# Optimization experiments

Measured on AMD Instinct MI355X. Metric: run time of the kernel, lower is better.

The kernel has to match this reference:

```python
import jax, jax.numpy as jnp
import numpy as np

N_NODES = 50000
N_EDGES = 800000
NODE_DIM = 128
EDGE_DIM = 32
HID = 64
NEG_SLOPE = 0.2  # PyG GATConv default


def _gat_layer(x, src, dst, edge_attr, W, We, a_src, a_dst, a_edge, b, n_nodes):
    """PyG GATConv with heads=1, add_self_loops=True, fill_value='mean'."""
    h = x @ W                      # [N, H] node transform (bias=False in PyG)
    he = edge_attr @ We            # [E, H] edge transform
    # self-loop edge attr = mean of incoming edge_attr per node; linearity lets
    # us take the segment-mean of the transformed he instead.
    deg = jax.ops.segment_sum(jnp.ones((src.shape[0],), h.dtype), dst, num_segments=n_nodes)
    he_loop = jax.ops.segment_sum(he, dst, num_segments=n_nodes) / jnp.maximum(deg, 1.0)[:, None]
    loop = jnp.arange(n_nodes)
    src_a = jnp.concatenate([src, loop])
    dst_a = jnp.concatenate([dst, loop])
    he_a = jnp.concatenate([he, he_loop], axis=0)
    s_src = h @ a_src              # [N]
    s_dst = h @ a_dst              # [N]
    logits = jax.nn.leaky_relu(s_src[src_a] + s_dst[dst_a] + he_a @ a_edge, NEG_SLOPE)
    # segment softmax over destination nodes (every node has a self loop)
    m = jax.ops.segment_max(logits, dst_a, num_segments=n_nodes)
    ex = jnp.exp(logits - m[dst_a])
    denom = jax.ops.segment_sum(ex, dst_a, num_segments=n_nodes)
    alpha = ex / denom[dst_a]
    out = jax.ops.segment_sum(alpha[:, None] * h[src_a], dst_a, num_segments=n_nodes)
    return out + b


def setup_inputs() -> dict:
    key = jax.random.key(0)
    ks = jax.random.split(key, 20)
    s = 0.05
    inp = {
        "x": jax.random.normal(ks[0], (N_NODES, NODE_DIM), jnp.float32),
        "edge_index": jax.random.randint(ks[1], (2, N_EDGES), 0, N_NODES, jnp.int64 if jax.config.jax_enable_x64 else jnp.int32).astype(jnp.int32),
        "edge_attr": jax.random.normal(ks[2], (N_EDGES, EDGE_DIM), jnp.float32),
        "W1": jax.random.normal(ks[3], (NODE_DIM, HID)) * s,
        "We1": jax.random.normal(ks[4], (EDGE_DIM, HID)) * s,
        "as1": jax.random.normal(ks[5], (HID,)) * s,
        "ad1": jax.random.normal(ks[6], (HID,)) * s,
        "ae1": jax.random.normal(ks[7], (HID,)) * s,
        "b1": jnp.zeros((HID,)),
        "W2": jax.random.normal(ks[8], (HID, HID)) * s,
        "We2": jax.random.normal(ks[9], (EDGE_DIM, HID)) * s,
        "as2": jax.random.normal(ks[10], (HID,)) * s,
        "ad2": jax.random.normal(ks[11], (HID,)) * s,
        "ae2": jax.random.normal(ks[12], (HID,)) * s,
        "b2": jnp.zeros((HID,)),
        "Wc1": jax.random.normal(ks[13], (2 * HID + EDGE_DIM, HID)) * s,
        "bc1": jnp.zeros((HID,)),
        "Wc2": jax.random.normal(ks[14], (HID, 1)) * s,
        "bc2": jnp.zeros((1,)),
    }
    return inp


def reference(x, edge_index, edge_attr, W1, We1, as1, ad1, ae1, b1,
              W2, We2, as2, ad2, ae2, b2, Wc1, bc1, Wc2, bc2):
    n_nodes = x.shape[0]
    row, col = edge_index[0], edge_index[1]
    x1 = jax.nn.relu(_gat_layer(x, row, col, edge_attr, W1, We1, as1, ad1, ae1, b1, n_nodes))
    x2 = jax.nn.relu(_gat_layer(x1, row, col, edge_attr, W2, We2, as2, ad2, ae2, b2, n_nodes))
    ef = jnp.concatenate([x2[row], x2[col], edge_attr], axis=-1)  # [E, 2H+De]
    h = jax.nn.relu(ef @ Wc1 + bc1)
    return (h @ Wc2 + bc2)[:, 0]
```

## Files before the change

### kernel.cpp

```cpp
#include <hip/hip_runtime.h>
#include <hip/hip_bf16.h>

#define NODE_DIM 128
#define EDGE_DIM 32
#define HID 64
#define NEG_SLOPE 0.2f

typedef __attribute__((ext_vector_type(8))) short bf16x8;
typedef __attribute__((ext_vector_type(4))) float f32x4;


template <int CTRL, int RM, int BM>
__device__ __forceinline__ float dpp_mov(float v) {
    return __int_as_float(__builtin_amdgcn_update_dpp(
        __float_as_int(v), __float_as_int(v), CTRL, RM, BM, false));
}

__device__ __forceinline__ float wave_sum63(float v) {
    v += dpp_mov<0x111, 0xf, 0xf>(v);
    v += dpp_mov<0x112, 0xf, 0xf>(v);
    v += dpp_mov<0x114, 0xf, 0xe>(v);
    v += dpp_mov<0x118, 0xf, 0xc>(v);
    v += dpp_mov<0x142, 0xa, 0xf>(v);
    v += dpp_mov<0x143, 0xc, 0xf>(v);
    return v;
}

__device__ __forceinline__ float row16_sum15(float v) {
    v += dpp_mov<0x111, 0xf, 0xf>(v);
    v += dpp_mov<0x112, 0xf, 0xf>(v);
    v += dpp_mov<0x114, 0xf, 0xe>(v);
    v += dpp_mov<0x118, 0xf, 0xc>(v);
    return v;
}

__device__ __forceinline__ float bcast63(float v) {
    return __int_as_float(__builtin_amdgcn_readlane(__float_as_int(v), 63));
}

__device__ __forceinline__ unsigned short f2bf(float f) {
    unsigned u = __float_as_uint(f);
    unsigned r = (u + 0x7fffu + ((u >> 16) & 1u)) >> 16;
    return (unsigned short)r;
}
__device__ __forceinline__ float bf2f(unsigned short h) {
    return __uint_as_float(((unsigned)h) << 16);
}


__global__ void k_count_rank_t12(const int* __restrict__ col, int* __restrict__ deg,
                                 int* __restrict__ rank, const float* __restrict__ ea,
                                 const float* __restrict__ wea1,
                                 const float* __restrict__ wea2,
                                 float2* __restrict__ t12, int E) {
    int e = blockIdx.x * 256 + threadIdx.x;
    if (e >= E) return;
    rank[e] = atomicAdd(&deg[col[e]], 1);
    const float4* e4 = (const float4*)(ea + (size_t)e * EDGE_DIM);
    const float4* w1 = (const float4*)wea1;
    const float4* w2 = (const float4*)wea2;
    float t1 = 0.f, t2 = 0.f;
#pragma unroll
    for (int k = 0; k < EDGE_DIM / 4; k++) {
        float4 v = e4[k], a = w1[k], b = w2[k];
        t1 += v.x * a.x + v.y * a.y + v.z * a.z + v.w * a.w;
        t2 += v.x * b.x + v.y * b.y + v.z * b.z + v.w * b.w;
    }
    t12[e] = make_float2(t1, t2);
}

#define SCAN_B 256
__global__ void k_scan1(const int* __restrict__ deg, int* __restrict__ tmp,
                        int* __restrict__ bsum, int N) {
    __shared__ int s[SCAN_B];
    int i = blockIdx.x * SCAN_B + threadIdx.x;
    int v = (i < N) ? deg[i] : 0;
    s[threadIdx.x] = v;
    __syncthreads();
    for (int o = 1; o < SCAN_B; o <<= 1) {
        int t = (threadIdx.x >= o) ? s[threadIdx.x - o] : 0;
        __syncthreads();
        s[threadIdx.x] += t;
        __syncthreads();
    }
    if (i < N) tmp[i] = s[threadIdx.x];
    if (threadIdx.x == SCAN_B - 1) bsum[blockIdx.x] = s[threadIdx.x];
}

__global__ void k_scan2(int* __restrict__ bsum, int nb) {
    __shared__ int s[SCAN_B];
    int v = (threadIdx.x < nb) ? bsum[threadIdx.x] : 0;
    s[threadIdx.x] = v;
    __syncthreads();
    for (int o = 1; o < SCAN_B; o <<= 1) {
        int t = (threadIdx.x >= o) ? s[threadIdx.x - o] : 0;
        __syncthreads();
        s[threadIdx.x] += t;
        __syncthreads();
    }
    if (threadIdx.x < nb) bsum[threadIdx.x] = s[threadIdx.x] - v;
}

__global__ void k_scan3(const int* __restrict__ tmp, const int* __restrict__ deg,
                        const int* __restrict__ bsum, int* __restrict__ off, int N) {
    int i = blockIdx.x * SCAN_B + threadIdx.x;
    if (i < N) off[i] = tmp[i] - deg[i] + bsum[blockIdx.x];
}

__global__ void k_wea2(const float* __restrict__ We1, const float* __restrict__ ae1,
                       const float* __restrict__ We2, const float* __restrict__ ae2,
                       float* __restrict__ wea1, float* __restrict__ wea2) {
    int t = threadIdx.x;
    const float* We = (t < 32) ? We1 : We2;
    const float* ae = (t < 32) ? ae1 : ae2;
    float* o = (t < 32) ? wea1 : wea2;
    int k = t & 31;
    float s = 0.f;
#pragma unroll
    for (int j = 0; j < HID; j++) s += We[k * HID + j] * ae[j];
    o[k] = s;
}

__global__ void k_fill_pack(const int* __restrict__ row, const int* __restrict__ col,
                            const int* __restrict__ off, const int* __restrict__ rank,
                            const float2* __restrict__ t12, const float* __restrict__ ss1,
                            float4* __restrict__ pk, int E) {
    int e = blockIdx.x * 256 + threadIdx.x;
    if (e >= E) return;
    int dn = col[e];
    int p = off[dn] + rank[e];
    float2 t = t12[e];
    int sr = row[e];
    pk[p] = make_float4(t.x, t.y, __int_as_float(sr), t.x + ss1[sr]);
}

template <int K, int NT, bool ATT, bool PQ>
__global__ __launch_bounds__(256) void k_gemm_mfma(
    const float* __restrict__ X, const float* __restrict__ W,
    const float* __restrict__ as_, const float* __restrict__ ad_,
    unsigned short* __restrict__ H, unsigned short* __restrict__ H2,
    float* __restrict__ ss, float* __restrict__ sd, int N) {
    constexpr int KC = K / 32;
    int wv = threadIdx.x >> 6, lane = threadIdx.x & 63;
    int g = lane >> 4, li = lane & 15;
    bf16x8 bhi[KC][NT], blo[KC][NT];
#pragma unroll
    for (int c = 0; c < KC; c++)
#pragma unroll
        for (int t = 0; t < NT; t++)
#pragma unroll
            for (int j = 0; j < 8; j++) {
                int k = 32 * c + 8 * g + j;
                size_t idx = (size_t)(k + ((PQ && t >= 4) ? HID : 0)) * HID + 16 * (t & 3) + li;
                float w = W[idx];
                unsigned short h = f2bf(w);
                bhi[c][t][j] = (short)h;
                blo[c][t][j] = (short)f2bf(w - bf2f(h));
            }
    float asl[NT], adl[NT];
    if (ATT) {
#pragma unroll
        for (int t = 0; t < NT; t++) {
            asl[t] = as_[16 * t + li];
            adl[t] = ad_[16 * t + li];
        }
    }
    int ntile = (N + 15) >> 4;
    for (int tb = blockIdx.x * 4 + wv; tb < ntile; tb += gridDim.x * 4) {
        int node = tb * 16 + li;
        if (node >= N) node = N - 1;
        const float* xrow = X + (size_t)node * K;
        bf16x8 ahi[KC], alo[KC];
#pragma unroll
        for (int c = 0; c < KC; c++) {
            float4 a0 = *(const float4*)(xrow + 32 * c + 8 * g);
            float4 a1 = *(const float4*)(xrow + 32 * c + 8 * g + 4);
            float xv[8] = {a0.x, a0.y, a0.z, a0.w, a1.x, a1.y, a1.z, a1.w};
#pragma unroll
            for (int j = 0; j < 8; j++) {
                unsigned short h = f2bf(xv[j]);
                ahi[c][j] = (short)h;
                alo[c][j] = (short)f2bf(xv[j] - bf2f(h));
            }
        }
        f32x4 acc[NT];
#pragma unroll
        for (int t = 0; t < NT; t++) acc[t] = (f32x4){0.f, 0.f, 0.f, 0.f};
#pragma unroll
        for (int c = 0; c < KC; c++) {
#pragma unroll
            for (int t = 0; t < NT; t++)
                acc[t] = __builtin_amdgcn_mfma_f32_16x16x32_bf16(ahi[c], bhi[c][t], acc[t], 0, 0, 0);
#pragma unroll
            for (int t = 0; t < NT; t++)
                acc[t] = __builtin_amdgcn_mfma_f32_16x16x32_bf16(ahi[c], blo[c][t], acc[t], 0, 0, 0);
#pragma unroll
            for (int t = 0; t < NT; t++)
                acc[t] = __builtin_amdgcn_mfma_f32_16x16x32_bf16(alo[c], bhi[c][t], acc[t], 0, 0, 0);
        }
        int nbase = tb * 16 + 4 * g;
#pragma unroll
        for (int t = 0; t < NT; t++) {
            unsigned short* dst = (PQ && t >= 4) ? H2 : H;
            int cofs = 16 * (t & 3) + li;
#pragma unroll
            for (int r = 0; r < 4; r++) {
                int n = nbase + r;
                if (n < N) dst[(size_t)n * HID + cofs] = f2bf(acc[t][r]);
            }
        }
        if (ATT) {
#pragma unroll
            for (int r = 0; r < 4; r++) {
                float s1 = 0.f, s2 = 0.f;
#pragma unroll
                for (int t = 0; t < NT; t++) {
                    s1 += acc[t][r] * asl[t];
                    s2 += acc[t][r] * adl[t];
                }
                s1 = row16_sum15(s1);
                s2 = row16_sum15(s2);
                int n = nbase + r;
                if (li == 15 && n < N) {
                    ss[n] = s1;
                    sd[n] = s2;
                }
            }
        }
    }
}

template <bool FOLD>
__global__ __launch_bounds__(256) void k_aggregate(
    const unsigned short* __restrict__ H, const float* __restrict__ ss,
    const float* __restrict__ sd, const float4* __restrict__ pk,
    const int* __restrict__ off, const int* __restrict__ deg,
    const float* __restrict__ b, float* __restrict__ Xo, int N) {
    __shared__ __align__(16) float2 sh[4][64];
    int wv = threadIdx.x >> 6, lane = threadIdx.x & 63;
    int g = lane >> 4, li = lane & 15;
    int n = blockIdx.x * 4 + wv;
    if (n >= N) return;
    int st = off[n], d = deg[n];
    float sdn = sd[n];
    float tsum = 0.f, dsum = 0.f;
    float a0 = 0.f, a1 = 0.f, a2 = 0.f, a3 = 0.f;
    for (int base = 0; base < d; base += 64) {
        int i = base + lane;
        float w = 0.f;
        int s = 0;
        if (i < d) {
            float4 p = pk[st + i];
            s = __float_as_int(p.z);
            float z;
            if (FOLD) {
                tsum += p.x;
                z = p.w + sdn;
            } else {
                tsum += p.y;
                z = ss[s] + sdn + p.y;
            }
            float l = z > 0.f ? z : NEG_SLOPE * z;
            w = __expf(l);
            dsum += w;
        }
        sh[wv][lane] = make_float2(w, __int_as_float(s));
        int cnt = d - base;
        if (cnt > 64) cnt = 64;
        for (int j = 0; j < cnt; j += 4) {
            int jg = j + g;
            float2 pr = (jg < cnt) ? sh[wv][jg] : make_float2(0.f, 0.f);
            const ushort4 hv =
                *(const ushort4*)(H + (size_t)__float_as_int(pr.y) * HID + 4 * li);
            a0 += pr.x * bf2f(hv.x);
            a1 += pr.x * bf2f(hv.y);
            a2 += pr.x * bf2f(hv.z);
            a3 += pr.x * bf2f(hv.w);
        }
    }
    tsum = bcast63(wave_sum63(tsum));
    dsum = bcast63(wave_sum63(dsum));
    float tloop = tsum / (float)(d > 1 ? d : 1);
    float zs = ss[n] + sdn + tloop;
    float lself = zs > 0.f ? zs : NEG_SLOPE * zs;
    float wself = __expf(lself);
    dsum += wself;
    if (g == 0) {
        const ushort4 hv = *(const ushort4*)(H + (size_t)n * HID + 4 * li);
        a0 += wself * bf2f(hv.x);
        a1 += wself * bf2f(hv.y);
        a2 += wself * bf2f(hv.z);
        a3 += wself * bf2f(hv.w);
    }
    a0 += __shfl_xor(a0, 16, 64); a0 += __shfl_xor(a0, 32, 64);
    a1 += __shfl_xor(a1, 16, 64); a1 += __shfl_xor(a1, 32, 64);
    a2 += __shfl_xor(a2, 16, 64); a2 += __shfl_xor(a2, 32, 64);
    a3 += __shfl_xor(a3, 16, 64); a3 += __shfl_xor(a3, 32, 64);
    if (g == 0) {
        float4 bv = *(const float4*)(b + 4 * li);
        float4 o;
        o.x = fmaxf(a0 / dsum + bv.x, 0.f);
        o.y = fmaxf(a1 / dsum + bv.y, 0.f);
        o.z = fmaxf(a2 / dsum + bv.z, 0.f);
        o.w = fmaxf(a3 / dsum + bv.w, 0.f);
        *(float4*)(Xo + (size_t)n * HID + 4 * li) = o;
    }
}

__global__ __launch_bounds__(256) void k_edge_final_mfma(
    const unsigned short* __restrict__ P, const unsigned short* __restrict__ Q,
    const float* __restrict__ ea, const int* __restrict__ row,
    const int* __restrict__ col, const float* __restrict__ Wc1,
    const float* __restrict__ bc1, const float* __restrict__ Wc2,
    const float* __restrict__ bc2, float* __restrict__ out, int E) {
    int wv = threadIdx.x >> 6, lane = threadIdx.x & 63;
    int g = lane >> 4, li = lane & 15;
    bf16x8 bfrag[4];
#pragma unroll
    for (int t = 0; t < 4; t++) {
#pragma unroll
        for (int j = 0; j < 8; j++)
            bfrag[t][j] = (short)f2bf(Wc1[(size_t)(2 * HID + 8 * g + j) * HID + 4 * li + t]);
    }
    float bcv[4], wc2v[4];
#pragma unroll
    for (int t = 0; t < 4; t++) {
        bcv[t] = bc1[4 * li + t];
        wc2v[t] = Wc2[4 * li + t];
    }
    float bc2v = bc2[0];
    int ntile = (E + 15) >> 4;
    for (int tb = blockIdx.x * 4 + wv; tb < ntile; tb += gridDim.x * 4) {
        int eb = tb << 4;
        int ae_e = eb + li;
        if (ae_e >= E) ae_e = E - 1;
        const float4* ap = (const float4*)(ea + (size_t)ae_e * EDGE_DIM + 8 * g);
        float4 a0 = ap[0], a1 = ap[1];
        bf16x8 afrag;
        afrag[0] = (short)f2bf(a0.x); afrag[1] = (short)f2bf(a0.y);
        afrag[2] = (short)f2bf(a0.z); afrag[3] = (short)f2bf(a0.w);
        afrag[4] = (short)f2bf(a1.x); afrag[5] = (short)f2bf(a1.y);
        afrag[6] = (short)f2bf(a1.z); afrag[7] = (short)f2bf(a1.w);
        f32x4 acc[4];
#pragma unroll
        for (int t = 0; t < 4; t++) {
            f32x4 z = {0.f, 0.f, 0.f, 0.f};
            acc[t] = __builtin_amdgcn_mfma_f32_16x16x32_bf16(afrag, bfrag[t], z, 0, 0, 0);
        }
        int e0 = eb + 4 * g;
        int rr[4], cc[4];
        if (e0 + 3 < E) {
            int4 rv = *(const int4*)(row + e0);
            int4 cv = *(const int4*)(col + e0);
            rr[0] = rv.x; rr[1] = rv.y; rr[2] = rv.z; rr[3] = rv.w;
            cc[0] = cv.x; cc[1] = cv.y; cc[2] = cv.z; cc[3] = cv.w;
        } else {
            for (int r = 0; r < 4; r++) {
                int e = e0 + r; if (e >= E) e = E - 1;
                rr[r] = row[e]; cc[r] = col[e];
            }
        }
        float pe[4];
#pragma unroll
        for (int r = 0; r < 4; r++) {
            const ushort4 pv = *(const ushort4*)(P + (size_t)rr[r] * HID + 4 * li);
            const ushort4 qv = *(const ushort4*)(Q + (size_t)cc[r] * HID + 4 * li);
            float h0 = acc[0][r] + bf2f(pv.x) + bf2f(qv.x) + bcv[0];
            float h1 = acc[1][r] + bf2f(pv.y) + bf2f(qv.y) + bcv[1];
            float h2 = acc[2][r] + bf2f(pv.z) + bf2f(qv.z) + bcv[2];
            float h3 = acc[3][r] + bf2f(pv.w) + bf2f(qv.w) + bcv[3];
            pe[r] = fmaxf(h0, 0.f) * wc2v[0] + fmaxf(h1, 0.f) * wc2v[1] +
                    fmaxf(h2, 0.f) * wc2v[2] + fmaxf(h3, 0.f) * wc2v[3];
        }
#pragma unroll
        for (int r = 0; r < 4; r++) pe[r] = row16_sum15(pe[r]);
        if (li == 15) {
            if (e0 + 3 < E) {
                *(float4*)(out + e0) =
                    make_float4(pe[0] + bc2v, pe[1] + bc2v, pe[2] + bc2v, pe[3] + bc2v);
            } else {
                for (int r = 0; r < 4; r++)
                    if (e0 + r < E) out[e0 + r] = pe[r] + bc2v;
            }
        }
    }
}


extern "C" void kernel_launch(void* const* d_in, const int* in_sizes, int n_in,
                              void* d_out, int out_size, void* d_ws, size_t ws_size,
                              hipStream_t stream) {
    const float* x = (const float*)d_in[0];
    const int* eidx = (const int*)d_in[1];
    const float* ea = (const float*)d_in[2];
    const float* W1 = (const float*)d_in[3];
    const float* We1 = (const float*)d_in[4];
    const float* as1 = (const float*)d_in[5];
    const float* ad1 = (const float*)d_in[6];
    const float* ae1 = (const float*)d_in[7];
    const float* b1 = (const float*)d_in[8];
    const float* W2 = (const float*)d_in[9];
    const float* We2 = (const float*)d_in[10];
    const float* as2 = (const float*)d_in[11];
    const float* ad2 = (const float*)d_in[12];
    const float* ae2 = (const float*)d_in[13];
    const float* b2 = (const float*)d_in[14];
    const float* Wc1 = (const float*)d_in[15];
    const float* bc1 = (const float*)d_in[16];
    const float* Wc2 = (const float*)d_in[17];
    const float* bc2 = (const float*)d_in[18];
    float* out = (float*)d_out;

    const int N = in_sizes[0] / NODE_DIM;
    const int E = in_sizes[1] / 2;
    const int* row = eidx;
    const int* col = eidx + E;

    char* ws = (char*)d_ws;
    size_t o = 0;
    auto carve = [&](size_t bytes) -> char* {
        char* p = ws + o;
        o += (bytes + 255) & ~(size_t)255;
        return p;
    };
    int* deg = (int*)carve((size_t)N * 4);
    int* off = (int*)carve((size_t)N * 4);
    int* tmp = (int*)carve((size_t)N * 4);
    int* bsum = (int*)carve(SCAN_B * 4);
    int* rank = (int*)carve((size_t)E * 4);
    float2* t12 = (float2*)carve((size_t)E * 8);
    float4* pk12 = (float4*)carve((size_t)E * 16);
    float* wea1 = (float*)carve(EDGE_DIM * 4);
    float* wea2 = (float*)carve(EDGE_DIM * 4);
    float* ssrc = (float*)carve((size_t)N * 4);
    float* sdst = (float*)carve((size_t)N * 4);
    unsigned short* hbuf = (unsigned short*)carve((size_t)N * HID * 2);
    unsigned short* pbuf = (unsigned short*)carve((size_t)N * HID * 2);
    float* x1 = (float*)carve((size_t)N * HID * 4);
    float* x2 = (float*)carve((size_t)N * HID * 4);
    (void)ws_size;

    const int gE = (E + 255) / 256;
    const int gN256 = (N + SCAN_B - 1) / SCAN_B;
    const int gN4 = (N + 3) / 4;
    const int gT = ((N + 15) / 16 + 3) / 4;

    (void)hipMemsetAsync(deg, 0, (size_t)N * 4, stream);
    k_wea2<<<1, 64, 0, stream>>>(We1, ae1, We2, ae2, wea1, wea2);
    k_count_rank_t12<<<gE, 256, 0, stream>>>(col, deg, rank, ea, wea1, wea2, t12, E);
    k_scan1<<<gN256, SCAN_B, 0, stream>>>(deg, tmp, bsum, N);
    k_scan2<<<1, SCAN_B, 0, stream>>>(bsum, gN256);
    k_scan3<<<gN256, SCAN_B, 0, stream>>>(tmp, deg, bsum, off, N);

    k_gemm_mfma<NODE_DIM, 4, true, false><<<gT, 256, 0, stream>>>(
        x, W1, as1, ad1, hbuf, nullptr, ssrc, sdst, N);
    k_fill_pack<<<gE, 256, 0, stream>>>(row, col, off, rank, t12, ssrc, pk12, E);

    k_aggregate<true><<<gN4, 256, 0, stream>>>(hbuf, ssrc, sdst, pk12, off, deg, b1, x1, N);

    k_gemm_mfma<HID, 4, true, false><<<gT, 256, 0, stream>>>(
        x1, W2, as2, ad2, hbuf, nullptr, ssrc, sdst, N);
    k_aggregate<false><<<gN4, 256, 0, stream>>>(hbuf, ssrc, sdst, pk12, off, deg, b2, x2, N);

    k_gemm_mfma<HID, 8, false, true><<<gT, 256, 0, stream>>>(
        x2, Wc1, nullptr, nullptr, pbuf, hbuf, nullptr, nullptr, N);
    k_edge_final_mfma<<<2048, 256, 0, stream>>>(pbuf, hbuf, ea, row, col, Wc1, bc1, Wc2, bc2, out, E);
}
```

Baseline: 413.4 us.

## Move edge-attr projection into fill kernel and prefetch next tile in edge MLP

```diff
diff --git a/kernel.cpp b/kernel.cpp
--- a/kernel.cpp
+++ b/kernel.cpp
@@ -48,25 +48,11 @@
 }
 
 
-__global__ void k_count_rank_t12(const int* __restrict__ col, int* __restrict__ deg,
-                                 int* __restrict__ rank, const float* __restrict__ ea,
-                                 const float* __restrict__ wea1,
-                                 const float* __restrict__ wea2,
-                                 float2* __restrict__ t12, int E) {
+__global__ void k_count_rank(const int* __restrict__ col, int* __restrict__ deg,
+                             int* __restrict__ rank, int E) {
     int e = blockIdx.x * 256 + threadIdx.x;
     if (e >= E) return;
     rank[e] = atomicAdd(&deg[col[e]], 1);
-    const float4* e4 = (const float4*)(ea + (size_t)e * EDGE_DIM);
-    const float4* w1 = (const float4*)wea1;
-    const float4* w2 = (const float4*)wea2;
-    float t1 = 0.f, t2 = 0.f;
-#pragma unroll
-    for (int k = 0; k < EDGE_DIM / 4; k++) {
-        float4 v = e4[k], a = w1[k], b = w2[k];
-        t1 += v.x * a.x + v.y * a.y + v.z * a.z + v.w * a.w;
-        t2 += v.x * b.x + v.y * b.y + v.z * b.z + v.w * b.w;
-    }
-    t12[e] = make_float2(t1, t2);
 }
 
 #define SCAN_B 256
@@ -121,17 +107,27 @@
     o[k] = s;
 }
 
-__global__ void k_fill_pack(const int* __restrict__ row, const int* __restrict__ col,
-                            const int* __restrict__ off, const int* __restrict__ rank,
-                            const float2* __restrict__ t12, const float* __restrict__ ss1,
-                            float4* __restrict__ pk, int E) {
+__global__ void k_t12_fill(const int* __restrict__ row, const int* __restrict__ col,
+                           const int* __restrict__ off, const int* __restrict__ rank,
+                           const float* __restrict__ ea, const float* __restrict__ wea1,
+                           const float* __restrict__ wea2, const float* __restrict__ ss1,
+                           float4* __restrict__ pk, int E) {
     int e = blockIdx.x * 256 + threadIdx.x;
     if (e >= E) return;
+    const float4* e4 = (const float4*)(ea + (size_t)e * EDGE_DIM);
+    const float4* w1 = (const float4*)wea1;
+    const float4* w2 = (const float4*)wea2;
+    float t1 = 0.f, t2 = 0.f;
+#pragma unroll
+    for (int k = 0; k < EDGE_DIM / 4; k++) {
+        float4 v = e4[k], a = w1[k], b = w2[k];
+        t1 += v.x * a.x + v.y * a.y + v.z * a.z + v.w * a.w;
+        t2 += v.x * b.x + v.y * b.y + v.z * b.z + v.w * b.w;
+    }
     int dn = col[e];
     int p = off[dn] + rank[e];
-    float2 t = t12[e];
     int sr = row[e];
-    pk[p] = make_float4(t.x, t.y, __int_as_float(sr), t.x + ss1[sr]);
+    pk[p] = make_float4(t1, t2, __int_as_float(sr), t1 + ss1[sr]);
 }
 
 template <int K, int NT, bool ATT, bool PQ>
@@ -330,25 +326,19 @@
     }
     float bc2v = bc2[0];
     int ntile = (E + 15) >> 4;
-    for (int tb = blockIdx.x * 4 + wv; tb < ntile; tb += gridDim.x * 4) {
+    int stride = gridDim.x * 4;
+    int tb = blockIdx.x * 4 + wv;
+    if (tb >= ntile) return;
+
+    float4 a0, a1;
+    int rr[4], cc[4];
+    {
         int eb = tb << 4;
         int ae_e = eb + li;
         if (ae_e >= E) ae_e = E - 1;
         const float4* ap = (const float4*)(ea + (size_t)ae_e * EDGE_DIM + 8 * g);
-        float4 a0 = ap[0], a1 = ap[1];
-        bf16x8 afrag;
-        afrag[0] = (short)f2bf(a0.x); afrag[1] = (short)f2bf(a0.y);
-        afrag[2] = (short)f2bf(a0.z); afrag[3] = (short)f2bf(a0.w);
-        afrag[4] = (short)f2bf(a1.x); afrag[5] = (short)f2bf(a1.y);
-        afrag[6] = (short)f2bf(a1.z); afrag[7] = (short)f2bf(a1.w);
-        f32x4 acc[4];
-#pragma unroll
-        for (int t = 0; t < 4; t++) {
-            f32x4 z = {0.f, 0.f, 0.f, 0.f};
-            acc[t] = __builtin_amdgcn_mfma_f32_16x16x32_bf16(afrag, bfrag[t], z, 0, 0, 0);
-        }
+        a0 = ap[0]; a1 = ap[1];
         int e0 = eb + 4 * g;
-        int rr[4], cc[4];
         if (e0 + 3 < E) {
             int4 rv = *(const int4*)(row + e0);
             int4 cv = *(const int4*)(col + e0);
@@ -360,15 +350,59 @@
                 rr[r] = row[e]; cc[r] = col[e];
             }
         }
+    }
+
+    while (true) {
+        int e0 = (tb << 4) + 4 * g;
+        ushort4 pv[4], qv[4];
+#pragma unroll
+        for (int r = 0; r < 4; r++) {
+            pv[r] = *(const ushort4*)(P + (size_t)rr[r] * HID + 4 * li);
+            qv[r] = *(const ushort4*)(Q + (size_t)cc[r] * HID + 4 * li);
+        }
+        int tn = tb + stride;
+        bool hasnext = tn < ntile;
+        float4 n0 = a0, n1 = a1;
+        int nr[4], nc[4];
+#pragma unroll
+        for (int r = 0; r < 4; r++) { nr[r] = rr[r]; nc[r] = cc[r]; }
+        if (hasnext) {
+            int eb = tn << 4;
+            int ae_e = eb + li;
+            if (ae_e >= E) ae_e = E - 1;
+            const float4* ap = (const float4*)(ea + (size_t)ae_e * EDGE_DIM + 8 * g);
+            n0 = ap[0]; n1 = ap[1];
+            int ne0 = eb + 4 * g;
+            if (ne0 + 3 < E) {
+                int4 rv = *(const int4*)(row + ne0);
+                int4 cv = *(const int4*)(col + ne0);
+                nr[0] = rv.x; nr[1] = rv.y; nr[2] = rv.z; nr[3] = rv.w;
+                nc[0] = cv.x; nc[1] = cv.y; nc[2] = cv.z; nc[3] = cv.w;
+            } else {
+                for (int r = 0; r < 4; r++) {
+                    int e = ne0 + r; if (e >= E) e = E - 1;
+                    nr[r] = row[e]; nc[r] = col[e];
+                }
+            }
+        }
+        bf16x8 afrag;
+        afrag[0] = (short)f2bf(a0.x); afrag[1] = (short)f2bf(a0.y);
+        afrag[2] = (short)f2bf(a0.z); afrag[3] = (short)f2bf(a0.w);
+        afrag[4] = (short)f2bf(a1.x); afrag[5] = (short)f2bf(a1.y);
+        afrag[6] = (short)f2bf(a1.z); afrag[7] = (short)f2bf(a1.w);
+        f32x4 acc[4];
+#pragma unroll
+        for (int t = 0; t < 4; t++) {
+            f32x4 z = {0.f, 0.f, 0.f, 0.f};
+            acc[t] = __builtin_amdgcn_mfma_f32_16x16x32_bf16(afrag, bfrag[t], z, 0, 0, 0);
+        }
         float pe[4];
 #pragma unroll
         for (int r = 0; r < 4; r++) {
-            const ushort4 pv = *(const ushort4*)(P + (size_t)rr[r] * HID + 4 * li);
-            const ushort4 qv = *(const ushort4*)(Q + (size_t)cc[r] * HID + 4 * li);
-            float h0 = acc[0][r] + bf2f(pv.x) + bf2f(qv.x) + bcv[0];
-            float h1 = acc[1][r] + bf2f(pv.y) + bf2f(qv.y) + bcv[1];
-            float h2 = acc[2][r] + bf2f(pv.z) + bf2f(qv.z) + bcv[2];
-            float h3 = acc[3][r] + bf2f(pv.w) + bf2f(qv.w) + bcv[3];
+            float h0 = acc[0][r] + bf2f(pv[r].x) + bf2f(qv[r].x) + bcv[0];
+            float h1 = acc[1][r] + bf2f(pv[r].y) + bf2f(qv[r].y) + bcv[1];
+            float h2 = acc[2][r] + bf2f(pv[r].z) + bf2f(qv[r].z) + bcv[2];
+            float h3 = acc[3][r] + bf2f(pv[r].w) + bf2f(qv[r].w) + bcv[3];
             pe[r] = fmaxf(h0, 0.f) * wc2v[0] + fmaxf(h1, 0.f) * wc2v[1] +
                     fmaxf(h2, 0.f) * wc2v[2] + fmaxf(h3, 0.f) * wc2v[3];
         }
@@ -383,6 +417,11 @@
                     if (e0 + r < E) out[e0 + r] = pe[r] + bc2v;
             }
         }
+        if (!hasnext) break;
+        tb = tn;
+        a0 = n0; a1 = n1;
+#pragma unroll
+        for (int r = 0; r < 4; r++) { rr[r] = nr[r]; cc[r] = nc[r]; }
     }
 }
 
@@ -428,7 +467,6 @@
     int* tmp = (int*)carve((size_t)N * 4);
     int* bsum = (int*)carve(SCAN_B * 4);
     int* rank = (int*)carve((size_t)E * 4);
-    float2* t12 = (float2*)carve((size_t)E * 8);
     float4* pk12 = (float4*)carve((size_t)E * 16);
     float* wea1 = (float*)carve(EDGE_DIM * 4);
     float* wea2 = (float*)carve(EDGE_DIM * 4);
@@ -447,14 +485,14 @@
 
     (void)hipMemsetAsync(deg, 0, (size_t)N * 4, stream);
     k_wea2<<<1, 64, 0, stream>>>(We1, ae1, We2, ae2, wea1, wea2);
-    k_count_rank_t12<<<gE, 256, 0, stream>>>(col, deg, rank, ea, wea1, wea2, t12, E);
+    k_count_rank<<<gE, 256, 0, stream>>>(col, deg, rank, E);
     k_scan1<<<gN256, SCAN_B, 0, stream>>>(deg, tmp, bsum, N);
     k_scan2<<<1, SCAN_B, 0, stream>>>(bsum, gN256);
     k_scan3<<<gN256, SCAN_B, 0, stream>>>(tmp, deg, bsum, off, N);
 
     k_gemm_mfma<NODE_DIM, 4, true, false><<<gT, 256, 0, stream>>>(
         x, W1, as1, ad1, hbuf, nullptr, ssrc, sdst, N);
-    k_fill_pack<<<gE, 256, 0, stream>>>(row, col, off, rank, t12, ssrc, pk12, E);
+    k_t12_fill<<<gE, 256, 0, stream>>>(row, col, off, rank, ea, wea1, wea2, ssrc, pk12, E);
 
     k_aggregate<true><<<gN4, 256, 0, stream>>>(hbuf, ssrc, sdst, pk12, off, deg, b1, x1, N);
 
```

After: 442.3 us. 7.0% more time.
